# Optimization experiments

Hardware: AMD Instinct MI355X
Metric: run time of the kernel (lower is better)

Reference implementation:

```python
import jax, jax.numpy as jnp
import numpy as np

B, NKP = 262144, 18
EPS = 1e-5


def setup_inputs() -> dict:
    key = jax.random.key(0)
    ks = jax.random.split(key, 24)
    coords = jax.random.uniform(ks[0], (B, NKP, 2), jnp.float32, 0.0, 200.0)
    missing = jax.random.bernoulli(ks[1], 0.15, (B, NKP))  # whole keypoint set to -1 sentinel
    input_cor = jnp.where(missing[:, :, None], -1.0, coords)
    train_mask = jax.random.bernoulli(ks[2], 0.3, (B, NKP * 2))
    r = lambda k, s: jax.random.normal(k, s, jnp.float32) * 0.1
    return {
        "input_cor": input_cor, "train_mask": train_mask,
        "conv1_w": r(ks[3], (10, 18, 1)), "conv1_b": r(ks[4], (10,)),
        "bn1_g": jnp.ones((10,)), "bn1_b": jnp.zeros((10,)),
        "bn1_m": r(ks[5], (10,)), "bn1_v": jax.random.uniform(ks[6], (10,), jnp.float32, 0.5, 1.5),
        "conv2_w": r(ks[7], (20, 10, 2)), "conv2_b": r(ks[8], (20,)),
        "bn2_g": jnp.ones((20,)), "bn2_b": jnp.zeros((20,)),
        "bn2_m": r(ks[9], (20,)), "bn2_v": jax.random.uniform(ks[10], (20,), jnp.float32, 0.5, 1.5),
        "conv3_w": r(ks[11], (30, 20, 2)), "conv3_b": r(ks[12], (30,)),
        "bn3_g": jnp.ones((30,)), "bn3_b": jnp.zeros((30,)),
        "bn3_m": r(ks[13], (30,)), "bn3_v": jax.random.uniform(ks[14], (30,), jnp.float32, 0.5, 1.5),
        "fc1_w": r(ks[15], (100, 60)), "fc1_b": r(ks[16], (100,)),
        "fc2_w": r(ks[17], (36, 100)), "fc2_b": r(ks[18], (36,)),
    }


def _conv1d(x, w, b, pad):
    y = jax.lax.conv_general_dilated(x, w, (1,), [(pad, pad)],
                                     dimension_numbers=("NCH", "OIH", "NCH"))
    return y + b[None, :, None]


def _bn(x, g, bt, m, v):
    return (x - m[None, :, None]) * (g / jnp.sqrt(v + EPS))[None, :, None] + bt[None, :, None]


def _dist(a, b):  # a,b: [B,2] -> [B]
    return jnp.sqrt(jnp.sum((a - b) ** 2, axis=-1))


def _part_loss(x, c, pred_dis, gt_dis, idxs):
    # valid iff x-coordinate of all three keypoints != -1 (as in the torch loop)
    valid = (c[:, idxs[0], 0] != -1) & (c[:, idxs[1], 0] != -1) & (c[:, idxs[2], 0] != -1)
    vf = valid.astype(x.dtype)
    n = vf.sum()
    s = jnp.sum((pred_dis - gt_dis) ** 2 * vf)
    return jnp.where(n > 0, s / jnp.maximum(n, 1.0), 0.0)


def reference(input_cor, train_mask,
              conv1_w, conv1_b, bn1_g, bn1_b, bn1_m, bn1_v,
              conv2_w, conv2_b, bn2_g, bn2_b, bn2_m, bn2_v,
              conv3_w, conv3_b, bn3_g, bn3_b, bn3_m, bn3_v,
              fc1_w, fc1_b, fc2_w, fc2_b):
    c = input_cor  # [B,18,2]
    Bn = c.shape[0]
    h = jax.nn.relu(_bn(_conv1d(c, conv1_w, conv1_b, 1), bn1_g, bn1_b, bn1_m, bn1_v))  # [B,10,4]
    h = jax.nn.relu(_bn(_conv1d(h, conv2_w, conv2_b, 0), bn2_g, bn2_b, bn2_m, bn2_v))  # [B,20,3]
    h = jax.nn.relu(_bn(_conv1d(h, conv3_w, conv3_b, 0), bn3_g, bn3_b, bn3_m, bn3_v))  # [B,30,2]
    h = h.reshape(Bn, 60)
    h = jax.nn.relu(h @ fc1_w.T + fc1_b)
    out = h @ fc2_w.T + fc2_b  # [B,36]

    gt = c.reshape(Bn, 36)
    mf = train_mask.astype(out.dtype)
    kp_loss = jnp.sum((out - gt) ** 2 * mf) / jnp.sum(mf)

    x = out.reshape(Bn, NKP, 2)

    # head: star pattern around keypoint 0 (faithful incl. original's use of x[:,15,0] in gt)
    head_pred = (_dist(x[:, 0], x[:, 14]) + _dist(x[:, 0], x[:, 15])) * 0.5
    head_gt = (_dist(c[:, 0], c[:, 14]) +
               jnp.sqrt((c[:, 0, 0] - x[:, 15, 0]) ** 2 + (c[:, 0, 1] - c[:, 15, 1]) ** 2)) * 0.5
    total = kp_loss + _part_loss(x, c, head_pred, head_gt, (0, 14, 15))

    # chain parts (a-b-c); gt second segment mixes x[:,c,0] (faithful to original)
    for a, b, cc in ((2, 3, 4), (5, 6, 7), (8, 9, 10), (11, 12, 13)):
        pred = (_dist(x[:, a], x[:, b]) + _dist(x[:, b], x[:, cc])) * 0.5
        gtd = (_dist(c[:, a], c[:, b]) +
               jnp.sqrt((c[:, b, 0] - x[:, cc, 0]) ** 2 + (c[:, b, 1] - c[:, cc, 1]) ** 2)) * 0.5
        total = total + _part_loss(x, c, pred, gtd, (a, b, cc))

    miss_mask = c != -1
    return x, total, miss_mask
```

## Files before the change

kernel.cpp:

```cpp
#include <hip/hip_runtime.h>
#include <hip/hip_bf16.h>

#define NB   1024
#define NT   256
#define BTOT 262144

typedef __attribute__((ext_vector_type(8))) short short8;
typedef __attribute__((ext_vector_type(4))) float f32x4;

__device__ __forceinline__ float relu_(float x) { return fmaxf(x, 0.0f); }

__device__ __forceinline__ short f2bf(float x) {
    unsigned u = __float_as_uint(x);
    return (short)((u + 0x7FFFu + ((u >> 16) & 1u)) >> 16);
}
__device__ __forceinline__ unsigned pk2bf(float a, float b) {
    return ((unsigned)(unsigned short)f2bf(a)) |
           (((unsigned)(unsigned short)f2bf(b)) << 16);
}

__device__ __forceinline__ void st_bf16(unsigned char* p, float x) {
    *(__hip_bfloat16*)p = __float2bfloat16(x);
}
__device__ __forceinline__ unsigned pkbf(float a, float b) {
    __hip_bfloat162 h = __float22bfloat162_rn(make_float2(a, b));
    return *(unsigned*)&h;
}
__device__ __forceinline__ short8 pack8(float a0,float a1,float a2,float a3,
                                        float a4,float a5,float a6,float a7) {
    uint4 v = make_uint4(pkbf(a0,a1), pkbf(a2,a3), pkbf(a4,a5), pkbf(a6,a7));
    return *(short8*)&v;
}

#define A0_DW    160
#define FRAGS_BYTE 768
#define PART_BYTE 47872
#define NFRAG 46

__global__ __launch_bounds__(256) void kp_setup(
    const float* __restrict__ w1, const float* __restrict__ b1,
    const float* __restrict__ g1, const float* __restrict__ bt1,
    const float* __restrict__ m1, const float* __restrict__ v1,
    const float* __restrict__ w2, const float* __restrict__ b2,
    const float* __restrict__ g2, const float* __restrict__ bt2,
    const float* __restrict__ m2, const float* __restrict__ v2,
    const float* __restrict__ w3, const float* __restrict__ b3,
    const float* __restrict__ g3, const float* __restrict__ bt3,
    const float* __restrict__ m3, const float* __restrict__ v3,
    const float* __restrict__ fw1, const float* __restrict__ fb1,
    const float* __restrict__ fw2, const float* __restrict__ fb2,
    float* __restrict__ wsB, short* __restrict__ frags)
{
    __shared__ float w1f[180], b1f[10], a0f[10];
    __shared__ float w2f[400], b2f[20];
    __shared__ float w3f[1200], b3f[30];
    const int t = threadIdx.x;

    if (t < 10) {
        float s = g1[t] * rsqrtf(v1[t] + 1e-5f);
        float bb = (b1[t] - m1[t]) * s + bt1[t];
        b1f[t] = bb; a0f[t] = relu_(bb);
        for (int i = 0; i < 18; ++i) w1f[t * 18 + i] = w1[t * 18 + i] * s;
    } else if (t >= 64 && t < 84) {
        int o = t - 64;
        float s = g2[o] * rsqrtf(v2[o] + 1e-5f);
        b2f[o] = (b2[o] - m2[o]) * s + bt2[o];
        for (int i = 0; i < 20; ++i) w2f[o * 20 + i] = w2[o * 20 + i] * s;
    } else if (t >= 128 && t < 158) {
        int o = t - 128;
        float s = g3[o] * rsqrtf(v3[o] + 1e-5f);
        b3f[o] = (b3[o] - m3[o]) * s + bt3[o];
        for (int i = 0; i < 40; ++i) w3f[o * 40 + i] = w3[o * 40 + i] * s;
    }
    __syncthreads();

    if (blockIdx.x == 0 && t < 5)
        ((unsigned*)wsB)[A0_DW + t] = pk2bf(a0f[2 * t], a0f[2 * t + 1]);

    for (int e = blockIdx.x * 256 + t; e < NFRAG * 512; e += gridDim.x * 256) {
        int frag = e >> 9, l = (e >> 3) & 63, j = e & 7;
        float val = 0.f;
        if (frag < 4) {
            int p = frag, nt = p >> 1, kt = p & 1;
            int k = kt * 32 + (l >> 4) * 8 + j, n = nt * 16 + (l & 15);
            if (n < 20) {
                int o = n % 10, pp = n / 10;
                if (k < 36) { int i = k >> 1, s = k & 1; if (s == pp) val = w1f[o * 18 + i]; }
                else if (k == 36) val = b1f[o];
            }
        } else if (frag < 12) {
            int p = frag - 4, nt = p >> 1, kt = p & 1;
            int k = kt * 32 + (l >> 4) * 8 + j, n = nt * 16 + (l & 15);
            if (n < 60) {
                int q = n / 20, o = n % 20;
                if (k < 40) { int pp = k / 10, i = k % 10, d = pp - q;
                              if (d == 0 || d == 1) val = w2f[o * 20 + i * 2 + d]; }
                else if (k == 40) val = b2f[o];
            }
        } else if (frag < 20) {
            int p = frag - 12, nt = p >> 1, kt = p & 1;
            int k = kt * 32 + (l >> 4) * 8 + j, n = nt * 16 + (l & 15);
            if (n < 60) {
                int q = n / 30, o = n % 30;
                if (k < 60) { int pp = k / 20, i = k % 20, d = pp - q;
                              if (d == 0 || d == 1) val = w3f[o * 40 + i * 2 + d]; }
                else if (k == 60) val = b3f[o];
            }
        } else if (frag < 34) {
            int p = frag - 20, n7 = p >> 1, kt = p & 1;
            int k = kt * 32 + (l >> 4) * 8 + j, col = n7 * 16 + (l & 15);
            if (col < 100) {
                if (k < 60) val = fw1[col * 60 + k];
                else if (k == 60) val = fb1[col];
            }
        } else {
            int p = frag - 34, n3 = p >> 2, kt = p & 3;
            int k = kt * 32 + (l >> 4) * 8 + j, col = n3 * 16 + (l & 15);
            if (col < 36) {
                if (k < 100) val = fw2[col * 100 + k];
                else if (k == 100) val = fb2[col];
            }
        }
        frags[e] = f2bf(val);
    }
}

__global__ __launch_bounds__(NT) void kp_main(
    const float* __restrict__ cin, const int* __restrict__ tmask,
    const float* __restrict__ wsB, const short* __restrict__ frags,
    float* __restrict__ xout, float* __restrict__ missout,
    float* __restrict__ partials)
{
    __shared__ __align__(16) unsigned char sOUT[NT * 88];
    __shared__ __align__(16) unsigned char sT1[4 * 16 * 144];
    __shared__ __align__(16) unsigned char sT2[4 * 16 * 144];

    const int t = threadIdx.x;
    const int lane = t & 63, wave = t >> 6;
    const unsigned lrow = (unsigned)(lane & 15);
    const unsigned lkg  = (unsigned)(lane >> 4);
    const unsigned wbase = (unsigned)(t & ~63);
    const short8* frg = (const short8*)frags;

    unsigned char* T1 = sT1 + wave * (16 * 144);
    unsigned char* T2 = sT2 + wave * (16 * 144);

    {
        const unsigned* a0p = (const unsigned*)wsB + A0_DW;
        uint4 A0q = *(const uint4*)a0p;
        unsigned A0e = a0p[4];
        if (lane < 16) {
            unsigned char* b = &T1[(unsigned)lane * 144];
            uint4 z4 = make_uint4(0u, 0u, 0u, 0u);
            *(uint4*)(b + 80)  = z4;
            *(uint4*)(b + 96)  = z4;
            *(uint4*)(b + 112) = z4;
            *(uint4*)(b + 128) = z4;
            *(unsigned*)(b + 80) = 0x00003F80u;
            *(uint4*)(b + 0)  = A0q;
            *(unsigned*)(b + 16) = A0e;
            *(unsigned*)(b + 60) = A0q.x;
            *(uint4*)(b + 64) = make_uint4(A0q.y, A0q.z, A0q.w, A0e);
            unsigned char* b2 = &T2[(unsigned)lane * 144];
            *(uint2*)(b2 + 120) = make_uint2(0u, 0u);
            *(uint4*)(b2 + 128) = z4;
        }
    }

    #pragma unroll 1
    for (int m = 0; m < 4; ++m) {
        const unsigned Rb = wbase + 16u * (unsigned)m;

        const float* crow = cin + (size_t)(blockIdx.x * NT + Rb + lrow) * 36;
        float4 qa = *(const float4*)(crow + 8 * lkg);
        float4 qb = *(const float4*)(crow + 8 * lkg + 4);
        float4 qc = *(const float4*)(crow + 32);
        short8 Aa = pack8(qa.x, qa.y, qa.z, qa.w, qb.x, qb.y, qb.z, qb.w);
        float sf = (lkg == 0u) ? 1.f : 0.f;
        short8 Ab = pack8(qc.x * sf, qc.y * sf, qc.z * sf, qc.w * sf, sf, 0.f, 0.f, 0.f);

        if (lane < 16)
            *(unsigned*)&T2[lane * 144 + 120] = 0x00003F80u;

        {
            f32x4 D1[2];
            #pragma unroll
            for (int nt = 0; nt < 2; ++nt) {
                D1[nt] = (f32x4){0.f, 0.f, 0.f, 0.f};
                D1[nt] = __builtin_amdgcn_mfma_f32_16x16x32_bf16(Aa, frg[(nt * 2 + 0) * 64 + lane], D1[nt], 0, 0, 0);
                D1[nt] = __builtin_amdgcn_mfma_f32_16x16x32_bf16(Ab, frg[(nt * 2 + 1) * 64 + lane], D1[nt], 0, 0, 0);
            }
            #pragma unroll
            for (int nt = 0; nt < 2; ++nt) {
                int n1 = nt * 16 + (int)lrow;
                if (n1 < 20) {
                    #pragma unroll
                    for (int i = 0; i < 4; ++i)
                        st_bf16(&T1[(4 * lkg + i) * 144 + (n1 + 10) * 2],
                                relu_(D1[nt][i]));
                }
            }
        }

        Aa = *(const short8*)&T1[lrow * 144 + lkg * 16u];
        Ab = *(const short8*)&T1[lrow * 144 + 64u + lkg * 16u];
        {
            f32x4 D2[4];
            #pragma unroll
            for (int nt = 0; nt < 4; ++nt) {
                D2[nt] = (f32x4){0.f, 0.f, 0.f, 0.f};
                D2[nt] = __builtin_amdgcn_mfma_f32_16x16x32_bf16(Aa, frg[(4 + nt * 2 + 0) * 64 + lane], D2[nt], 0, 0, 0);
                D2[nt] = __builtin_amdgcn_mfma_f32_16x16x32_bf16(Ab, frg[(4 + nt * 2 + 1) * 64 + lane], D2[nt], 0, 0, 0);
            }
            #pragma unroll
            for (int nt = 0; nt < 4; ++nt) {
                int n2 = nt * 16 + (int)lrow;
                if (n2 < 60) {
                    #pragma unroll
                    for (int i = 0; i < 4; ++i)
                        st_bf16(&T2[(4 * lkg + i) * 144 + n2 * 2],
                                relu_(D2[nt][i]));
                }
            }
        }

        Aa = *(const short8*)&T2[lrow * 144 + lkg * 16u];
        Ab = *(const short8*)&T2[lrow * 144 + 64u + lkg * 16u];
        {
            f32x4 D3[4];
            #pragma unroll
            for (int nt = 0; nt < 4; ++nt) {
                D3[nt] = (f32x4){0.f, 0.f, 0.f, 0.f};
                D3[nt] = __builtin_amdgcn_mfma_f32_16x16x32_bf16(Aa, frg[(12 + nt * 2 + 0) * 64 + lane], D3[nt], 0, 0, 0);
                D3[nt] = __builtin_amdgcn_mfma_f32_16x16x32_bf16(Ab, frg[(12 + nt * 2 + 1) * 64 + lane], D3[nt], 0, 0, 0);
            }
            #pragma unroll
            for (int nt = 0; nt < 4; ++nt) {
                int n3 = nt * 16 + (int)lrow;
                if (n3 < 60) {
                    int o = (n3 >= 30) ? n3 - 30 : n3;
                    int kf = 2 * o + (n3 >= 30 ? 1 : 0);
                    #pragma unroll
                    for (int i = 0; i < 4; ++i)
                        st_bf16(&T2[(4 * lkg + i) * 144 + kf * 2],
                                relu_(D3[nt][i]));
                }
            }
        }

        short8 Fa = *(const short8*)&T2[lrow * 144 + lkg * 16u];
        short8 Fb = *(const short8*)&T2[lrow * 144 + 64u + lkg * 16u];
        f32x4 acc2[3];
        #pragma unroll
        for (int n = 0; n < 3; ++n) acc2[n] = (f32x4){0.f, 0.f, 0.f, 0.f};

        #pragma unroll
        for (int h = 0; h < 2; ++h) {
            #pragma unroll
            for (int nn = 0; nn < 4; ++nn) {
                const int n = 4 * h + nn;
                f32x4 a1v = (f32x4){0.f, 0.f, 0.f, 0.f};
                if (n < 7) {
                    a1v = __builtin_amdgcn_mfma_f32_16x16x32_bf16(Fa, frg[(20 + n * 2 + 0) * 64 + lane], a1v, 0, 0, 0);
                    a1v = __builtin_amdgcn_mfma_f32_16x16x32_bf16(Fb, frg[(20 + n * 2 + 1) * 64 + lane], a1v, 0, 0, 0);
                }
                #pragma unroll
                for (int i = 0; i < 4; ++i) {
                    float zv = (n < 7) ? relu_(a1v[i]) : 0.f;
                    if (n == 6 && (int)lrow == 4) zv = 1.f;
                    st_bf16(&T2[(4 * lkg + i) * 144 + (16 * nn + (int)lrow) * 2], zv);
                }
            }
            #pragma unroll
            for (int q = 0; q < 2; ++q) {
                const int kt = 2 * h + q;
                short8 Az = *(const short8*)&T2[lrow * 144 + (unsigned)(q * 64) + lkg * 16u];
                #pragma unroll
                for (int n = 0; n < 3; ++n)
                    acc2[n] = __builtin_amdgcn_mfma_f32_16x16x32_bf16(Az, frg[(34 + n * 4 + kt) * 64 + lane], acc2[n], 0, 0, 0);
            }
        }

        #pragma unroll
        for (int n = 0; n < 3; ++n) {
            const int col = 16 * n + (int)lrow;
            if (col < 36) {
                #pragma unroll
                for (int i = 0; i < 4; ++i)
                    st_bf16(&sOUT[(Rb + 4 * lkg + i) * 88 + col * 2],
                            acc2[n][i]);
            }
        }
    }

    const float* cp = cin + (size_t)(blockIdx.x * NT + t) * 36;
    float sp[5], np[5];
    {
        unsigned w0  = *(const unsigned*)&sOUT[t * 88 + 0];
        unsigned w28 = *(const unsigned*)&sOUT[t * 88 + 56];
        unsigned w30 = *(const unsigned*)&sOUT[t * 88 + 60];
        float o0x = __uint_as_float(w0 << 16),  o0y = __uint_as_float(w0 & 0xFFFF0000u);
        float o28 = __uint_as_float(w28 << 16), o29 = __uint_as_float(w28 & 0xFFFF0000u);
        float o30 = __uint_as_float(w30 << 16), o31 = __uint_as_float(w30 & 0xFFFF0000u);
        float2 c0  = *(const float2*)(cp + 0);
        float2 c28 = *(const float2*)(cp + 28);
        float2 c30 = *(const float2*)(cp + 30);
        float dxa = o0x - o28, dya = o0y - o29;
        float dxb = o0x - o30, dyb = o0y - o31;
        float pred = 0.5f * (sqrtf(dxa*dxa + dya*dya) + sqrtf(dxb*dxb + dyb*dyb));
        float cxa = c0.x - c28.x, cya = c0.y - c28.y;
        float gxa = c0.x - o30,   gya = c0.y - c30.y;
        float gt = 0.5f * (sqrtf(cxa*cxa + cya*cya) + sqrtf(gxa*gxa + gya*gya));
        float vf = (c0.x != -1.f && c28.x != -1.f && c30.x != -1.f) ? 1.f : 0.f;
        float e = pred - gt;
        sp[0] = e * e * vf; np[0] = vf;
    }
    #pragma unroll
    for (int p = 0; p < 4; ++p) {
        const int a = 2 + 3 * p;
        unsigned wA = *(const unsigned*)&sOUT[t * 88 + 4 * a + 0];
        unsigned wB = *(const unsigned*)&sOUT[t * 88 + 4 * a + 4];
        unsigned wC = *(const unsigned*)&sOUT[t * 88 + 4 * a + 8];
        float oax = __uint_as_float(wA << 16), oay = __uint_as_float(wA & 0xFFFF0000u);
        float obx = __uint_as_float(wB << 16), oby = __uint_as_float(wB & 0xFFFF0000u);
        float ocx = __uint_as_float(wC << 16), ocy = __uint_as_float(wC & 0xFFFF0000u);
        float2 ca = *(const float2*)(cp + 2 * a);
        float2 cb = *(const float2*)(cp + 2 * a + 2);
        float2 cc2 = *(const float2*)(cp + 2 * a + 4);
        float dxa = oax - obx, dya = oay - oby;
        float dxb = obx - ocx, dyb = oby - ocy;
        float pred = 0.5f * (sqrtf(dxa*dxa + dya*dya) + sqrtf(dxb*dxb + dyb*dyb));
        float cxa = ca.x - cb.x, cya = ca.y - cb.y;
        float gxa = cb.x - ocx,  gya = cb.y - cc2.y;
        float gt = 0.5f * (sqrtf(cxa*cxa + cya*cya) + sqrtf(gxa*gxa + gya*gya));
        float vf = (ca.x != -1.f && cb.x != -1.f && cc2.x != -1.f) ? 1.f : 0.f;
        float e = pred - gt;
        sp[p + 1] = e * e * vf; np[p + 1] = vf;
    }

    __syncthreads();

    const size_t blkBase = (size_t)blockIdx.x * (NT * 36);
    const float4* cin4 = (const float4*)(cin + blkBase);
    const int4*   tm4  = (const int4*)(tmask + blkBase);
    float4*       x4   = (float4*)(xout + blkBase);
    float*        mo   = missout + blkBase;

    float s1 = 0.f, s2 = 0.f;
    #pragma unroll
    for (int i = 0; i < 9; ++i) {
        int g4 = i * NT + t;
        unsigned g = 4u * (unsigned)g4;
        unsigned row = g / 36u;
        unsigned col = g - row * 36u;
        uint2 w = *(const uint2*)&sOUT[row * 88u + col * 2u];
        float4 xv;
        xv.x = __uint_as_float(w.x << 16);
        xv.y = __uint_as_float(w.x & 0xFFFF0000u);
        xv.z = __uint_as_float(w.y << 16);
        xv.w = __uint_as_float(w.y & 0xFFFF0000u);
        float4 cv = cin4[g4];
        int4   mv = tm4[g4];
        x4[g4] = xv;
        mo[g + 0] = (cv.x != -1.f) ? 1.f : 0.f;
        mo[g + 1] = (cv.y != -1.f) ? 1.f : 0.f;
        mo[g + 2] = (cv.z != -1.f) ? 1.f : 0.f;
        mo[g + 3] = (cv.w != -1.f) ? 1.f : 0.f;
        float m0 = (float)mv.x, m1_ = (float)mv.y, m2_ = (float)mv.z, m3_ = (float)mv.w;
        float d0 = xv.x - cv.x, d1 = xv.y - cv.y, d2 = xv.z - cv.z, d3 = xv.w - cv.w;
        s1 += d0*d0*m0 + d1*d1*m1_ + d2*d2*m2_ + d3*d3*m3_;
        s2 += m0 + m1_ + m2_ + m3_;
    }

    float rv[12] = { s1, s2, sp[0], np[0], sp[1], np[1],
                     sp[2], np[2], sp[3], np[3], sp[4], np[4] };
    #pragma unroll
    for (int v = 0; v < 12; ++v) {
        #pragma unroll
        for (int off = 32; off > 0; off >>= 1)
            rv[v] += __shfl_down(rv[v], off, 64);
    }
    if (lane == 0) {
        float* sw = (float*)(sT1 + wave * (16 * 144));
        #pragma unroll
        for (int v = 0; v < 12; ++v) sw[v] = rv[v];
    }
    __syncthreads();
    if (t < 12) {
        float s = 0.f;
        #pragma unroll
        for (int w = 0; w < 4; ++w) s += ((const float*)(sT1 + w * (16 * 144)))[t];
        partials[blockIdx.x * 12 + t] = s;
    }
}

__global__ __launch_bounds__(256) void kp_fin(const float* __restrict__ partials,
                                              float* __restrict__ total_out)
{
    __shared__ float sred[4][12];
    const int t = threadIdx.x;
    float rv[12];
    #pragma unroll
    for (int v = 0; v < 12; ++v) rv[v] = 0.f;
    for (int b = t; b < NB; b += 256) {
        #pragma unroll
        for (int v = 0; v < 12; ++v) rv[v] += partials[b * 12 + v];
    }
    #pragma unroll
    for (int v = 0; v < 12; ++v) {
        #pragma unroll
        for (int off = 32; off > 0; off >>= 1)
            rv[v] += __shfl_down(rv[v], off, 64);
    }
    const int wave = t >> 6, lane = t & 63;
    if (lane == 0) {
        #pragma unroll
        for (int v = 0; v < 12; ++v) sred[wave][v] = rv[v];
    }
    __syncthreads();
    if (t == 0) {
        float acc[12];
        #pragma unroll
        for (int v = 0; v < 12; ++v)
            acc[v] = sred[0][v] + sred[1][v] + sred[2][v] + sred[3][v];
        float total = acc[0] / acc[1];
        #pragma unroll
        for (int p = 0; p < 5; ++p) {
            float s = acc[2 + 2 * p], n = acc[3 + 2 * p];
            total += (n > 0.f) ? (s / fmaxf(n, 1.f)) : 0.f;
        }
        total_out[0] = total;
    }
}

extern "C" void kernel_launch(void* const* d_in, const int* in_sizes, int n_in,
                              void* d_out, int out_size, void* d_ws, size_t ws_size,
                              hipStream_t stream)
{
    const float* cin   = (const float*)d_in[0];
    const int*   tmask = (const int*)  d_in[1];
    const float* w1  = (const float*)d_in[2];
    const float* b1  = (const float*)d_in[3];
    const float* g1  = (const float*)d_in[4];
    const float* bt1 = (const float*)d_in[5];
    const float* m1  = (const float*)d_in[6];
    const float* v1  = (const float*)d_in[7];
    const float* w2  = (const float*)d_in[8];
    const float* b2  = (const float*)d_in[9];
    const float* g2  = (const float*)d_in[10];
    const float* bt2 = (const float*)d_in[11];
    const float* m2  = (const float*)d_in[12];
    const float* v2  = (const float*)d_in[13];
    const float* w3  = (const float*)d_in[14];
    const float* b3  = (const float*)d_in[15];
    const float* g3  = (const float*)d_in[16];
    const float* bt3 = (const float*)d_in[17];
    const float* m3  = (const float*)d_in[18];
    const float* v3  = (const float*)d_in[19];
    const float* fw1 = (const float*)d_in[20];
    const float* fb1 = (const float*)d_in[21];
    const float* fw2 = (const float*)d_in[22];
    const float* fb2 = (const float*)d_in[23];

    float* xout     = (float*)d_out;
    float* total    = (float*)d_out + (size_t)BTOT * 36;
    float* missout  = total + 1;

    float* wsB      = (float*)d_ws;
    short* frags    = (short*)((char*)d_ws + FRAGS_BYTE);
    float* partials = (float*)((char*)d_ws + PART_BYTE);

    kp_setup<<<8, 256, 0, stream>>>(
        w1, b1, g1, bt1, m1, v1,
        w2, b2, g2, bt2, m2, v2,
        w3, b3, g3, bt3, m3, v3,
        fw1, fb1, fw2, fb2, wsB, frags);

    kp_main<<<NB, NT, 0, stream>>>(cin, tmask, wsB, frags,
        xout, missout, partials);

    kp_fin<<<1, 256, 0, stream>>>(partials, total);
}
```

Before: 56.97 us.

## Interleave intermediate activation layout to pack bf16 LDS stores and permute weight fragments

Reorders the K dimension of each layer's weight fragments so that MFMA outputs from several N-tiles can be written to LDS as packed 32/64-bit bf16 stores (interleaved columns) instead of many scattered 16-bit stores with branches. It also drops the per-iteration bias-ones store in T2 by folding the constant-one column into the packed write, and simplifies the T1 setup. The permutation logic in the setup kernel must exactly match the new interleaved layout, which is a correctness risk.

```diff
diff --git a/kernel.cpp b/kernel.cpp
--- a/kernel.cpp
+++ b/kernel.cpp
@@ -19,12 +19,12 @@
            (((unsigned)(unsigned short)f2bf(b)) << 16);
 }
 
-__device__ __forceinline__ void st_bf16(unsigned char* p, float x) {
-    *(__hip_bfloat16*)p = __float2bfloat16(x);
-}
 __device__ __forceinline__ unsigned pkbf(float a, float b) {
     __hip_bfloat162 h = __float22bfloat162_rn(make_float2(a, b));
     return *(unsigned*)&h;
+}
+__device__ __forceinline__ void st_bf16(unsigned char* p, float x) {
+    *(__hip_bfloat16*)p = __float2bfloat16(x);
 }
 __device__ __forceinline__ short8 pack8(float a0,float a1,float a2,float a3,
                                         float a4,float a5,float a6,float a7) {
@@ -89,36 +89,48 @@
                 else if (k == 36) val = b1f[o];
             }
         } else if (frag < 12) {
-            int p = frag - 4, nt = p >> 1, kt = p & 1;
-            int k = kt * 32 + (l >> 4) * 8 + j, n = nt * 16 + (l & 15);
+            int p = frag - 4, nt_ = p >> 1, kt = p & 1;
+            int kp = kt * 32 + (l >> 4) * 8 + j, n = nt_ * 16 + (l & 15);
             if (n < 60) {
-                int q = n / 20, o = n % 20;
-                if (k < 40) { int pp = k / 10, i = k % 10, d = pp - q;
-                              if (d == 0 || d == 1) val = w2f[o * 20 + i * 2 + d]; }
-                else if (k == 40) val = b2f[o];
+                int lk = -1;
+                if (kp < 32) { int s = kp & 1, r = kp >> 1;
+                               lk = (s == 0) ? 10 + r : (r < 4 ? 26 + r : -1); }
+                else if (kp < 42) lk = kp - 32;
+                else if (kp < 52) lk = 30 + (kp - 42);
+                else if (kp == 52) lk = 40;
+                if (lk >= 0) {
+                    int q = n / 20, o = n % 20;
+                    if (lk < 40) { int pp = lk / 10, i = lk % 10, d = pp - q;
+                                   if (d == 0 || d == 1) val = w2f[o * 20 + i * 2 + d]; }
+                    else val = b2f[o];
+                }
             }
         } else if (frag < 20) {
-            int p = frag - 12, nt = p >> 1, kt = p & 1;
-            int k = kt * 32 + (l >> 4) * 8 + j, n = nt * 16 + (l & 15);
+            int p = frag - 12, nt_ = p >> 1, kt = p & 1;
+            int kp = kt * 32 + (l >> 4) * 8 + j, n = nt_ * 16 + (l & 15);
             if (n < 60) {
+                int n2 = 16 * (kp & 3) + (kp >> 2);
                 int q = n / 30, o = n % 30;
-                if (k < 60) { int pp = k / 20, i = k % 20, d = pp - q;
-                              if (d == 0 || d == 1) val = w3f[o * 40 + i * 2 + d]; }
-                else if (k == 60) val = b3f[o];
+                if (n2 < 60) { int pp = n2 / 20, i = n2 % 20, d = pp - q;
+                               if (d == 0 || d == 1) val = w3f[o * 40 + i * 2 + d]; }
+                else if (n2 == 60) val = b3f[o];
             }
         } else if (frag < 34) {
             int p = frag - 20, n7 = p >> 1, kt = p & 1;
-            int k = kt * 32 + (l >> 4) * 8 + j, col = n7 * 16 + (l & 15);
+            int kp = kt * 32 + (l >> 4) * 8 + j, col = n7 * 16 + (l & 15);
             if (col < 100) {
-                if (k < 60) val = fw1[col * 60 + k];
-                else if (k == 60) val = fb1[col];
+                int n3 = 16 * (kp & 3) + (kp >> 2);
+                if (n3 < 60) { int kf = 2 * (n3 % 30) + (n3 / 30);
+                               val = fw1[col * 60 + kf]; }
+                else if (n3 == 60) val = fb1[col];
             }
         } else {
-            int p = frag - 34, n3 = p >> 2, kt = p & 3;
-            int k = kt * 32 + (l >> 4) * 8 + j, col = n3 * 16 + (l & 15);
+            int p = frag - 34, n3_ = p >> 2, kt = p & 3;
+            int kp = kt * 32 + (l >> 4) * 8 + j, col = n3_ * 16 + (l & 15);
             if (col < 36) {
-                if (k < 100) val = fw2[col * 100 + k];
-                else if (k == 100) val = fb2[col];
+                int jj = 64 * (kp >> 6) + 16 * ((kp & 63) & 3) + ((kp & 63) >> 2);
+                if (jj < 100) val = fw2[col * 100 + jj];
+                else if (jj == 100) val = fb2[col];
             }
         }
         frags[e] = f2bf(val);
@@ -150,20 +162,11 @@
         uint4 A0q = *(const uint4*)a0p;
         unsigned A0e = a0p[4];
         if (lane < 16) {
-            unsigned char* b = &T1[(unsigned)lane * 144];
-            uint4 z4 = make_uint4(0u, 0u, 0u, 0u);
-            *(uint4*)(b + 80)  = z4;
-            *(uint4*)(b + 96)  = z4;
-            *(uint4*)(b + 112) = z4;
-            *(uint4*)(b + 128) = z4;
-            *(unsigned*)(b + 80) = 0x00003F80u;
-            *(uint4*)(b + 0)  = A0q;
-            *(unsigned*)(b + 16) = A0e;
-            *(unsigned*)(b + 60) = A0q.x;
-            *(uint4*)(b + 64) = make_uint4(A0q.y, A0q.z, A0q.w, A0e);
-            unsigned char* b2 = &T2[(unsigned)lane * 144];
-            *(uint2*)(b2 + 120) = make_uint2(0u, 0u);
-            *(uint4*)(b2 + 128) = z4;
+            unsigned char* b = &T1[(unsigned)lane * 144 + 64];
+            *(uint4*)(b +  0) = A0q;
+            *(uint4*)(b + 16) = make_uint4(A0e, A0q.x, A0q.y, A0q.z);
+            *(uint4*)(b + 32) = make_uint4(A0q.w, A0e, 0x00003F80u, 0u);
+            *(uint4*)(b + 48) = make_uint4(0u, 0u, 0u, 0u);
         }
     }
 
@@ -179,9 +182,6 @@
         float sf = (lkg == 0u) ? 1.f : 0.f;
         short8 Ab = pack8(qc.x * sf, qc.y * sf, qc.z * sf, qc.w * sf, sf, 0.f, 0.f, 0.f);
 
-        if (lane < 16)
-            *(unsigned*)&T2[lane * 144 + 120] = 0x00003F80u;
-
         {
             f32x4 D1[2];
             #pragma unroll
@@ -191,15 +191,9 @@
                 D1[nt] = __builtin_amdgcn_mfma_f32_16x16x32_bf16(Ab, frg[(nt * 2 + 1) * 64 + lane], D1[nt], 0, 0, 0);
             }
             #pragma unroll
-            for (int nt = 0; nt < 2; ++nt) {
-                int n1 = nt * 16 + (int)lrow;
-                if (n1 < 20) {
-                    #pragma unroll
-                    for (int i = 0; i < 4; ++i)
-                        st_bf16(&T1[(4 * lkg + i) * 144 + (n1 + 10) * 2],
-                                relu_(D1[nt][i]));
-                }
-            }
+            for (int i = 0; i < 4; ++i)
+                *(unsigned*)&T1[(4 * lkg + i) * 144 + lrow * 4] =
+                    pkbf(relu_(D1[0][i]), relu_(D1[1][i]));
         }
 
         Aa = *(const short8*)&T1[lrow * 144 + lkg * 16u];
@@ -213,14 +207,11 @@
                 D2[nt] = __builtin_amdgcn_mfma_f32_16x16x32_bf16(Ab, frg[(4 + nt * 2 + 1) * 64 + lane], D2[nt], 0, 0, 0);
             }
             #pragma unroll
-            for (int nt = 0; nt < 4; ++nt) {
-                int n2 = nt * 16 + (int)lrow;
-                if (n2 < 60) {
-                    #pragma unroll
-                    for (int i = 0; i < 4; ++i)
-                        st_bf16(&T2[(4 * lkg + i) * 144 + n2 * 2],
-                                relu_(D2[nt][i]));
-                }
+            for (int i = 0; i < 4; ++i) {
+                float e3 = (lrow == 12u) ? 1.0f : relu_(D2[3][i]);
+                uint2 wv = make_uint2(pkbf(relu_(D2[0][i]), relu_(D2[1][i])),
+                                      pkbf(relu_(D2[2][i]), e3));
+                *(uint2*)&T2[(4 * lkg + i) * 144 + lrow * 8] = wv;
             }
         }
 
@@ -235,16 +226,11 @@
                 D3[nt] = __builtin_amdgcn_mfma_f32_16x16x32_bf16(Ab, frg[(12 + nt * 2 + 1) * 64 + lane], D3[nt], 0, 0, 0);
             }
             #pragma unroll
-            for (int nt = 0; nt < 4; ++nt) {
-                int n3 = nt * 16 + (int)lrow;
-                if (n3 < 60) {
-                    int o = (n3 >= 30) ? n3 - 30 : n3;
-                    int kf = 2 * o + (n3 >= 30 ? 1 : 0);
-                    #pragma unroll
-                    for (int i = 0; i < 4; ++i)
-                        st_bf16(&T2[(4 * lkg + i) * 144 + kf * 2],
-                                relu_(D3[nt][i]));
-                }
+            for (int i = 0; i < 4; ++i) {
+                float e3 = (lrow == 12u) ? 1.0f : relu_(D3[3][i]);
+                uint2 wv = make_uint2(pkbf(relu_(D3[0][i]), relu_(D3[1][i])),
+                                      pkbf(relu_(D3[2][i]), e3));
+                *(uint2*)&T2[(4 * lkg + i) * 144 + lrow * 8] = wv;
             }
         }
 
@@ -257,18 +243,24 @@
         #pragma unroll
         for (int h = 0; h < 2; ++h) {
             #pragma unroll
-            for (int nn = 0; nn < 4; ++nn) {
-                const int n = 4 * h + nn;
-                f32x4 a1v = (f32x4){0.f, 0.f, 0.f, 0.f};
-                if (n < 7) {
-                    a1v = __builtin_amdgcn_mfma_f32_16x16x32_bf16(Fa, frg[(20 + n * 2 + 0) * 64 + lane], a1v, 0, 0, 0);
-                    a1v = __builtin_amdgcn_mfma_f32_16x16x32_bf16(Fb, frg[(20 + n * 2 + 1) * 64 + lane], a1v, 0, 0, 0);
+            for (int pr = 0; pr < 2; ++pr) {
+                const int n0 = 4 * h + 2 * pr;
+                const int n1 = n0 + 1;
+                f32x4 va = (f32x4){0.f, 0.f, 0.f, 0.f};
+                f32x4 vb = (f32x4){0.f, 0.f, 0.f, 0.f};
+                va = __builtin_amdgcn_mfma_f32_16x16x32_bf16(Fa, frg[(20 + n0 * 2 + 0) * 64 + lane], va, 0, 0, 0);
+                va = __builtin_amdgcn_mfma_f32_16x16x32_bf16(Fb, frg[(20 + n0 * 2 + 1) * 64 + lane], va, 0, 0, 0);
+                if (n1 < 7) {
+                    vb = __builtin_amdgcn_mfma_f32_16x16x32_bf16(Fa, frg[(20 + n1 * 2 + 0) * 64 + lane], vb, 0, 0, 0);
+                    vb = __builtin_amdgcn_mfma_f32_16x16x32_bf16(Fb, frg[(20 + n1 * 2 + 1) * 64 + lane], vb, 0, 0, 0);
                 }
                 #pragma unroll
                 for (int i = 0; i < 4; ++i) {
-                    float zv = (n < 7) ? relu_(a1v[i]) : 0.f;
-                    if (n == 6 && (int)lrow == 4) zv = 1.f;
-                    st_bf16(&T2[(4 * lkg + i) * 144 + (16 * nn + (int)lrow) * 2], zv);
+                    float z0 = relu_(va[i]);
+                    if (h == 1 && pr == 1 && lrow == 4u) z0 = 1.0f;
+                    float z1 = (n1 < 7) ? relu_(vb[i]) : 0.f;
+                    *(unsigned*)&T2[(4 * lkg + i) * 144 + lrow * 8 + 4 * pr] =
+                        pkbf(z0, z1);
                 }
             }
             #pragma unroll
```

New measurement: 55.60 us, median of 2. -2.4%, faster.
